# Performance work log

Measured on AMD Instinct MI355X. Metric: run time of the kernel, lower is better.

## Reference

```python
import jax, jax.numpy as jnp
import numpy as np

N = 50000      # nodes
E = 800000     # edges per relation
R = 2          # relations
L = 2          # conv layers
D = 128        # hidden / input channels
G = 64         # graphs in batch
C = 8          # num_classes


def setup_inputs() -> dict:
    key = jax.random.key(0)
    ks = jax.random.split(key, 6)
    x = jax.random.normal(ks[0], (N, D), dtype=jnp.float32)
    W = jax.random.normal(ks[1], (L, R, D, D), dtype=jnp.float32) * 0.05
    b = jnp.zeros((L, R, D), dtype=jnp.float32)
    lin_w = jax.random.normal(ks[2], (D, C), dtype=jnp.float32) * 0.05
    lin_b = jnp.zeros((C,), dtype=jnp.float32)
    edge_index = jax.random.randint(ks[3], (R, 2, E), 0, N, dtype=jnp.int32)
    batch = jnp.sort(jax.random.randint(ks[4], (N,), 0, G, dtype=jnp.int32))
    return {"x": x, "W": W, "b": b, "lin_w": lin_w, "lin_b": lin_b,
            "edge_index": edge_index, "batch": batch}


def _gcn_conv(x, src, dst, inv_sqrt_deg, W_r, b_r):
    """PyG GCNConv: symmetric-normalized aggregation with self loops.
    out[i] = sum_{j->i} d_i^-1/2 d_j^-1/2 (x_j W) + d_i^-1 (x_i W) + b
    where d includes the self loop (in-degree + 1)."""
    xw = x @ W_r                                   # [N, D]
    norm = inv_sqrt_deg[src] * inv_sqrt_deg[dst]   # [E]
    agg = jax.ops.segment_sum(xw[src] * norm[:, None], dst, num_segments=N)
    agg = agg + xw * (inv_sqrt_deg * inv_sqrt_deg)[:, None]  # self-loop msg
    return agg + b_r


def reference(x, W, b, lin_w, lin_b, edge_index, batch):
    # Pre-compute per-relation symmetric normalization (same for all layers).
    inv_sqrt_degs = []
    for r in range(R):
        dst = edge_index[r, 1]
        deg = jax.ops.segment_sum(jnp.ones((E,), x.dtype), dst, num_segments=N) + 1.0
        inv_sqrt_degs.append(jax.lax.rsqrt(deg))

    h = x
    for l in range(L):
        out = jnp.zeros((N, D), x.dtype)
        for r in range(R):  # HeteroConv aggr='sum' over relations
            out = out + _gcn_conv(h, edge_index[r, 0], edge_index[r, 1],
                                  inv_sqrt_degs[r], W[l, r], b[l, r])
        h = jax.nn.relu(out) if l < L - 1 else out

    # global_mean_pool over batch ids
    counts = jax.ops.segment_sum(jnp.ones((N,), x.dtype), batch, num_segments=G)
    sums = jax.ops.segment_sum(h, batch, num_segments=G)
    pooled = sums / jnp.maximum(counts, 1.0)[:, None]   # [G, D]
    # dropout(p=0.5) is identity in eval mode; final Linear
    return pooled @ lin_w + lin_b                        # [G, C]
```

## Files before the change

### kernel.cpp

```cpp
#include <hip/hip_runtime.h>
#include <math.h>

#define NN 50000
#define EE 800000
#define RR 2
#define LL 2
#define DD 128
#define GG 64
#define CCLS 8
#define NBUK 196
#define BCAP 6144
#define BCI2 14080

typedef unsigned int uint;
typedef unsigned short ushort;
typedef short bf16x8 __attribute__((ext_vector_type(8)));
typedef float f32x4 __attribute__((ext_vector_type(4)));
typedef float f32x2 __attribute__((ext_vector_type(2)));

#define OFF_H1    ((size_t)0)
#define OFF_WBT   ((size_t)12800000)
#define OFF_ISD   ((size_t)12931072)
#define OFF_RP    ((size_t)13331072)
#define OFF_CI    ((size_t)13732480)
#define OFF_ZERO  ((size_t)24771200)
#define OFF_BD    ((size_t)24805824)
#define OFF_XW    ((size_t)24805824)
#define ZO_GCUR 0
#define ZO_SUM  1600
#define ZO_CNT  34368
#define ZERO_BYTES 34624

static __device__ __forceinline__ ushort f2b(float f) {
  uint u = __float_as_uint(f);
  uint r = (u + 0x7fffu + ((u >> 16) & 1u)) >> 16;
  return (ushort)r;
}
static __device__ __forceinline__ float blo(uint u) { return __uint_as_float(u << 16); }
static __device__ __forceinline__ float bhi(uint u) { return __uint_as_float(u & 0xffff0000u); }

__global__ __launch_bounds__(256) void k_wprep(const float* __restrict__ W,
                                               ushort* __restrict__ WT) {
  int idx = blockIdx.x * 256 + threadIdx.x;
  int lr = idx >> 14;
  int rem = idx & 16383;
  int n = rem >> 7, k = rem & 127;
  WT[lr * 16384 + n * 128 + k] = f2b(W[lr * 16384 + k * 128 + n]);
}

__global__ __launch_bounds__(256) void k_part(const int* __restrict__ EI,
                                              int* __restrict__ gcur,
                                              uint* __restrict__ bdata) {
  __shared__ int hist[256];
  __shared__ int sbase[256];
  __shared__ int gbase[256];
  __shared__ int lcur[256];
  __shared__ uint stage[4096];
  __shared__ unsigned char bstage[4096];
  const int r = blockIdx.y;
  const int t = threadIdx.x;
  const int e0 = blockIdx.x * 4096;
  const int cnt = min(4096, EE - e0);
  hist[t] = 0;
  lcur[t] = 0;
  __syncthreads();

  int src[16], dst[16];
  bool val[4];
#pragma unroll
  for (int j = 0; j < 4; ++j) {
    int i4 = (j * 256 + t) * 4;
    val[j] = (i4 < cnt);
    if (val[j]) {
      int4 s4 = *(const int4*)(EI + (size_t)r * 2 * EE + e0 + i4);
      int4 d4 = *(const int4*)(EI + (size_t)r * 2 * EE + EE + e0 + i4);
      src[j * 4 + 0] = s4.x; src[j * 4 + 1] = s4.y; src[j * 4 + 2] = s4.z; src[j * 4 + 3] = s4.w;
      dst[j * 4 + 0] = d4.x; dst[j * 4 + 1] = d4.y; dst[j * 4 + 2] = d4.z; dst[j * 4 + 3] = d4.w;
#pragma unroll
      for (int i = 0; i < 4; ++i) atomicAdd(&hist[dst[j * 4 + i] >> 8], 1);
    }
  }
  __syncthreads();
  int hv = hist[t];
  if (t < NBUK && hv > 0)
    gbase[t] = atomicAdd(&gcur[r * NBUK + t], hv);
  else
    gbase[t] = 0;
  sbase[t] = hv;
  __syncthreads();
  for (int off = 1; off < 256; off <<= 1) {
    int u = (t >= off) ? sbase[t - off] : 0;
    __syncthreads();
    sbase[t] += u;
    __syncthreads();
  }
  int incl = sbase[t];
  hist[t] = incl - hv;
  __syncthreads();
#pragma unroll
  for (int j = 0; j < 4; ++j) {
    if (val[j]) {
#pragma unroll
      for (int i = 0; i < 4; ++i) {
        int d = dst[j * 4 + i];
        int b = d >> 8;
        int p = atomicAdd(&lcur[b], 1);
        int pos = hist[b] + p;
        stage[pos] = ((uint)src[j * 4 + i] << 8) | (uint)(d & 255);
        bstage[pos] = (unsigned char)b;
      }
    }
  }
  __syncthreads();
  for (int s = t; s < cnt; s += 256) {
    int b = (int)bstage[s];
    bdata[(size_t)(r * NBUK + b) * BCAP + gbase[b] + (s - hist[b])] = stage[s];
  }
}

__global__ __launch_bounds__(256) void k_csr(const uint* __restrict__ bdata,
                                             const int* __restrict__ gcur,
                                             float* __restrict__ isd,
                                             int* __restrict__ rps,
                                             int* __restrict__ rpc,
                                             int* __restrict__ ci) {
  __shared__ int lcnt0[256], lcnt1[256], lrp[256], lex[256], lng[256];
  __shared__ int lcurA[256], lcurB[256];
  __shared__ int cstage[BCI2];
  __shared__ int shtot;
  const int b = blockIdx.x;
  const int t = threadIdx.x;
  const int cnt0 = gcur[b];
  const int cnt1 = gcur[NBUK + b];
  const uint* bd0 = bdata + (size_t)b * BCAP;
  const uint* bd1 = bdata + (size_t)(NBUK + b) * BCAP;
  lcnt0[t] = 0; lcnt1[t] = 0; lcurA[t] = 0; lcurB[t] = 0;
  __syncthreads();
  for (int s = t; s < cnt0; s += 256) atomicAdd(&lcnt0[bd0[s] & 255u], 1);
  for (int s = t; s < cnt1; s += 256) atomicAdd(&lcnt1[bd1[s] & 255u], 1);
  __syncthreads();
  const int deg0 = lcnt0[t];
  const int deg1 = lcnt1[t];
  const int node = b * 256 + t;
  const int valid = (node < NN) ? 1 : 0;
  const int ng0 = valid ? ((deg0 + 8) >> 3) : 0;
  const int ng1 = valid ? ((deg1 + 8) >> 3) : 0;
  const int sz = (ng0 + ng1) << 3;
  lrp[t] = sz;
  __syncthreads();
  for (int off = 1; off < 256; off <<= 1) {
    int u = (t >= off) ? lrp[t - off] : 0;
    __syncthreads();
    lrp[t] += u;
    __syncthreads();
  }
  const int incl = lrp[t];
  if (t == 255) shtot = incl;
  const int ex = incl - sz;
  lex[t] = ex;
  lng[t] = ng0;
  __syncthreads();
  const int btot = shtot;
  if (t < 32) cstage[btot + t] = NN;
  rps[node] = b * BCI2 + ex;
  rpc[node] = ng0 | (ng1 << 16);
  if (valid) {
    isd[node] = rsqrtf((float)(deg0 + 1));
    isd[NN + node] = rsqrtf((float)(deg1 + 1));
    cstage[ex + deg0] = node;
    for (int p = deg0 + 1; p < (ng0 << 3); ++p) cstage[ex + p] = NN;
    const int ex1 = ex + (ng0 << 3);
    cstage[ex1 + deg1] = (NN + 1) + node;
    for (int p = deg1 + 1; p < (ng1 << 3); ++p) cstage[ex1 + p] = NN;
  }
  for (int s = t; s < cnt0; s += 256) {
    uint pr = bd0[s];
    int j = (int)(pr & 255u);
    int p = atomicAdd(&lcurA[j], 1);
    cstage[lex[j] + p] = (int)(pr >> 8);
  }
  for (int s = t; s < cnt1; s += 256) {
    uint pr = bd1[s];
    int j = (int)(pr & 255u);
    int p = atomicAdd(&lcurB[j], 1);
    cstage[lex[j] + (lng[j] << 3) + p] = (int)(pr >> 8) + (NN + 1);
  }
  __syncthreads();
  const int on = btot + 32;
  int* co = ci + (size_t)b * BCI2;
  for (int s = t; s < on; s += 256) co[s] = cstage[s];
}

#define AL_S 72
#define WT_S 136
template <int IN_BF16>
__global__ __launch_bounds__(256) void k_gemm(const void* __restrict__ Xv,
                                              const ushort* __restrict__ WTg,
                                              const float* __restrict__ isd,
                                              uint* __restrict__ Y) {
  __shared__ ushort WTl[128 * WT_S];
  __shared__ ushort Al[128 * AL_S];
  const int r = blockIdx.y;
  const int m0b = blockIdx.x * 128;
  const int t = threadIdx.x;
  const int w = t >> 6, L = t & 63, q = L >> 4, ln = L & 15;
  uint* Yr = Y + (size_t)r * (NN + 1) * 32;
  const ushort* WTr = WTg + (size_t)r * 16384;

#pragma unroll
  for (int i = 0; i < 8; ++i) {
    int g = t + i * 256;
    int n = g >> 4, k0 = (g & 15) * 8;
    *(uint4*)(&WTl[n * WT_S + k0]) = *(const uint4*)(WTr + n * 128 + k0);
  }

  f32x4 acc[2][8];
#pragma unroll
  for (int mt = 0; mt < 2; ++mt)
#pragma unroll
    for (int nt = 0; nt < 8; ++nt) {
      acc[mt][nt][0] = 0.f; acc[mt][nt][1] = 0.f;
      acc[mt][nt][2] = 0.f; acc[mt][nt][3] = 0.f;
    }

  for (int hh = 0; hh < 2; ++hh) {
    __syncthreads();
    {
      int row = t >> 1, ch = t & 1;
      int gm = m0b + row;
      ushort* dst = &Al[row * AL_S + ch * 32];
      if (gm < NN) {
        if (IN_BF16) {
          const uint4* xp = (const uint4*)((const ushort*)Xv + (size_t)gm * 128 + hh * 64 + ch * 32);
#pragma unroll
          for (int j = 0; j < 4; ++j) ((uint4*)dst)[j] = xp[j];
        } else {
          const float4* xp = (const float4*)((const float*)Xv + (size_t)gm * 128 + hh * 64 + ch * 32);
          ushort tmp[32];
#pragma unroll
          for (int j = 0; j < 8; ++j) {
            float4 v = xp[j];
            tmp[j * 4 + 0] = f2b(v.x); tmp[j * 4 + 1] = f2b(v.y);
            tmp[j * 4 + 2] = f2b(v.z); tmp[j * 4 + 3] = f2b(v.w);
          }
#pragma unroll
          for (int j = 0; j < 4; ++j) ((uint4*)dst)[j] = ((uint4*)tmp)[j];
        }
      } else {
        uint4 z = make_uint4(0, 0, 0, 0);
#pragma unroll
        for (int j = 0; j < 4; ++j) ((uint4*)dst)[j] = z;
      }
    }
    __syncthreads();
#pragma unroll
    for (int kk = 0; kk < 2; ++kk) {
      bf16x8 b0 = *(const bf16x8*)(&Al[(w * 32 + ln) * AL_S + kk * 32 + q * 8]);
      bf16x8 b1 = *(const bf16x8*)(&Al[(w * 32 + 16 + ln) * AL_S + kk * 32 + q * 8]);
#pragma unroll
      for (int nt = 0; nt < 8; ++nt) {
        bf16x8 a = *(const bf16x8*)(&WTl[(nt * 16 + ln) * WT_S + hh * 64 + kk * 32 + q * 8]);
        acc[0][nt] = __builtin_amdgcn_mfma_f32_16x16x32_bf16(a, b0, acc[0][nt], 0, 0, 0);
        acc[1][nt] = __builtin_amdgcn_mfma_f32_16x16x32_bf16(a, b1, acc[1][nt], 0, 0, 0);
      }
    }
  }
#pragma unroll
  for (int mt = 0; mt < 2; ++mt) {
    int m = m0b + w * 32 + mt * 16 + ln;
    if (m <= NN) {
      float sc = (m < NN) ? isd[r * NN + m] : 0.f;
      uint* yp = Yr + (size_t)m * 32;
#pragma unroll
      for (int nt = 0; nt < 8; ++nt) {
        f32x4 v = acc[mt][nt];
        uint u = __builtin_amdgcn_cvt_pk_fp8_f32(v[0] * sc, v[1] * sc, 0u, false);
        u = __builtin_amdgcn_cvt_pk_fp8_f32(v[2] * sc, v[3] * sc, u, true);
        yp[nt * 4 + q] = u;
      }
    }
  }
}

#define AGG_STEP()                                                           \
  {                                                                          \
    int s3 = ce0[ip]; ip += 8;                                               \
    uint4 u2 = *(const uint4*)(xw + ((size_t)((uint)s2 << 7) + cb));         \
    f32x2 v;                                                                 \
    v = __builtin_amdgcn_cvt_pk_f32_fp8(u0.x, false); acc[0] += v;           \
    v = __builtin_amdgcn_cvt_pk_f32_fp8(u0.x, true);  acc[1] += v;           \
    v = __builtin_amdgcn_cvt_pk_f32_fp8(u0.y, false); acc[2] += v;           \
    v = __builtin_amdgcn_cvt_pk_f32_fp8(u0.y, true);  acc[3] += v;           \
    v = __builtin_amdgcn_cvt_pk_f32_fp8(u0.z, false); acc[4] += v;           \
    v = __builtin_amdgcn_cvt_pk_f32_fp8(u0.z, true);  acc[5] += v;           \
    v = __builtin_amdgcn_cvt_pk_f32_fp8(u0.w, false); acc[6] += v;           \
    v = __builtin_amdgcn_cvt_pk_f32_fp8(u0.w, true);  acc[7] += v;           \
    u0 = u1; u1 = u2; s2 = s3;                                               \
  }

__global__ __launch_bounds__(256) void k_agg(const char* __restrict__ xw,
                                             const int* __restrict__ rps,
                                             const int* __restrict__ rpc,
                                             const int* __restrict__ ci,
                                             const float* __restrict__ isd,
                                             const float* __restrict__ bias,
                                             uint* __restrict__ hout, int relu_flag) {
  const int w = threadIdx.x >> 6;
  const int lane = threadIdx.x & 63;
  const int g = lane >> 3, c = lane & 7;
  const int wid = blockIdx.x * 4 + w;
  const int n0 = (wid >> 6) * 256 + (wid & 63) * 4;
  const size_t cb = (size_t)c * 16;

  const int m0 = rpc[n0], m1 = rpc[n0 + 1], m2 = rpc[n0 + 2], m3 = rpc[n0 + 3];
  const int* ce0 = ci + rps[n0];

  int ip = g;
  int s0 = ce0[ip]; ip += 8;
  int s1 = ce0[ip]; ip += 8;
  int s2 = ce0[ip]; ip += 8;
  uint4 u0 = *(const uint4*)(xw + ((size_t)((uint)s0 << 7) + cb));
  uint4 u1 = *(const uint4*)(xw + ((size_t)((uint)s1 << 7) + cb));

#pragma unroll
  for (int k = 0; k < 4; ++k) {
    const int node = n0 + k;
    const int meta_k = (k == 0) ? m0 : (k == 1) ? m1 : (k == 2) ? m2 : m3;
    const int ng0 = meta_k & 0xffff;
    const int ng1 = (meta_k >> 16) & 0xffff;
    const float di0 = isd[node];
    const float di1 = isd[NN + node];

    f32x2 acc[8];
#pragma unroll
    for (int j = 0; j < 8; ++j) { acc[j][0] = 0.f; acc[j][1] = 0.f; }
    for (int q = 0; q < ng0; ++q) AGG_STEP();
    f32x2 t8[8];
    {
      f32x2 d; d[0] = di0; d[1] = di0;
#pragma unroll
      for (int j = 0; j < 8; ++j) { t8[j] = acc[j] * d; acc[j][0] = 0.f; acc[j][1] = 0.f; }
    }
    for (int q = 0; q < ng1; ++q) AGG_STEP();
    {
      f32x2 d; d[0] = di1; d[1] = di1;
#pragma unroll
      for (int j = 0; j < 8; ++j) t8[j] += acc[j] * d;
    }

#pragma unroll
    for (int mask = 8; mask <= 32; mask <<= 1) {
#pragma unroll
      for (int j = 0; j < 8; ++j) {
        f32x2 o;
        o[0] = __shfl_xor(t8[j][0], mask);
        o[1] = __shfl_xor(t8[j][1], mask);
        t8[j] += o;
      }
    }

    if (g == 0 && node < NN) {
      const float4* p0 = (const float4*)(bias + c * 16);
      const float4* p1 = (const float4*)(bias + DD + c * 16);
      float o[16];
#pragma unroll
      for (int j = 0; j < 4; ++j) {
        float4 a = p0[j], bq = p1[j];
        o[4 * j + 0] = t8[2 * j][0] + a.x + bq.x;
        o[4 * j + 1] = t8[2 * j][1] + a.y + bq.y;
        o[4 * j + 2] = t8[2 * j + 1][0] + a.z + bq.z;
        o[4 * j + 3] = t8[2 * j + 1][1] + a.w + bq.w;
      }
      if (relu_flag) {
#pragma unroll
        for (int j = 0; j < 16; ++j) o[j] = fmaxf(o[j], 0.f);
      }
      uint pk[8];
#pragma unroll
      for (int j = 0; j < 8; ++j)
        pk[j] = (uint)f2b(o[2 * j]) | ((uint)f2b(o[2 * j + 1]) << 16);
      uint4* dst = (uint4*)(hout + (size_t)node * 64) + c * 2;
      dst[0] = make_uint4(pk[0], pk[1], pk[2], pk[3]);
      dst[1] = make_uint4(pk[4], pk[5], pk[6], pk[7]);
    }
  }
}

#define PCHUNK 32
__global__ __launch_bounds__(64) void k_pool(const uint* __restrict__ h,
                                             const int* __restrict__ batch,
                                             float* __restrict__ sums,
                                             int* __restrict__ counts) {
  int lane = threadIdx.x;
  int n0 = blockIdx.x * PCHUNK;
  int n1 = n0 + PCHUNK;
  if (n1 > NN) n1 = NN;
  if (n0 >= NN) return;
  float aLo = 0.f, aHi = 0.f;
  int cnt = 0;
  int g = batch[n0];
  uint u = h[(size_t)n0 * 64 + lane];
  for (int n = n0; n < n1; ++n) {
    uint unext = 0;
    int gnext = g;
    if (n + 1 < n1) {
      unext = h[(size_t)(n + 1) * 64 + lane];
      gnext = batch[n + 1];
    }
    aLo += blo(u);
    aHi += bhi(u);
    cnt++;
    if (n + 1 < n1 && gnext != g) {
      atomicAdd(&sums[g * DD + lane * 2], aLo);
      atomicAdd(&sums[g * DD + lane * 2 + 1], aHi);
      if (lane == 0) atomicAdd(&counts[g], cnt);
      aLo = 0.f; aHi = 0.f; cnt = 0;
      g = gnext;
    }
    u = unext;
  }
  atomicAdd(&sums[g * DD + lane * 2], aLo);
  atomicAdd(&sums[g * DD + lane * 2 + 1], aHi);
  if (lane == 0) atomicAdd(&counts[g], cnt);
}

__global__ __launch_bounds__(512) void k_final(const float* __restrict__ sums,
                                               const int* __restrict__ counts,
                                               const float* __restrict__ lin_w,
                                               const float* __restrict__ lin_b,
                                               float* __restrict__ out) {
  int t = threadIdx.x;
  int g = t >> 3, co = t & 7;
  float cnt = (float)counts[g];
  if (cnt < 1.f) cnt = 1.f;
  float inv = 1.f / cnt;
  float v = lin_b[co];
  for (int d = 0; d < DD; ++d) v += (sums[g * DD + d] * inv) * lin_w[d * CCLS + co];
  out[t] = v;
}

extern "C" void kernel_launch(void* const* d_in, const int* in_sizes, int n_in,
                              void* d_out, int out_size, void* d_ws, size_t ws_size,
                              hipStream_t stream) {
  (void)in_sizes; (void)n_in; (void)out_size; (void)ws_size;
  const float* x     = (const float*)d_in[0];
  const float* W     = (const float*)d_in[1];
  const float* b     = (const float*)d_in[2];
  const float* lin_w = (const float*)d_in[3];
  const float* lin_b = (const float*)d_in[4];
  const int*   EI    = (const int*)d_in[5];
  const int*   batch = (const int*)d_in[6];
  float* out = (float*)d_out;

  char* ws = (char*)d_ws;
  uint*   h1    = (uint*)(ws + OFF_H1);
  ushort* WbfT  = (ushort*)(ws + OFF_WBT);
  float*  isd   = (float*)(ws + OFF_ISD);
  int*    rps   = (int*)(ws + OFF_RP);
  int*    rpc   = rps + NBUK * 256;
  int*    ci    = (int*)(ws + OFF_CI);
  uint*   bdata = (uint*)(ws + OFF_BD);
  uint*   xw    = (uint*)(ws + OFF_XW);
  char*   zb    = ws + OFF_ZERO;
  int*    gcur  = (int*)(zb + ZO_GCUR);
  float*  sums  = (float*)(zb + ZO_SUM);
  int*    counts= (int*)(zb + ZO_CNT);

  (void)hipMemsetAsync(zb, 0, ZERO_BYTES, stream);

  k_wprep<<<256, 256, 0, stream>>>(W, WbfT);
  k_part<<<dim3((EE + 4095) / 4096, RR), 256, 0, stream>>>(EI, gcur, bdata);
  k_csr<<<NBUK, 256, 0, stream>>>(bdata, gcur, isd, rps, rpc, ci);

  for (int l = 0; l < LL; ++l) {
    const ushort* WTl_g = WbfT + (size_t)l * RR * DD * DD;
    if (l == 0)
      k_gemm<0><<<dim3((NN + 127) / 128, RR), 256, 0, stream>>>((const void*)x, WTl_g, isd, xw);
    else
      k_gemm<1><<<dim3((NN + 127) / 128, RR), 256, 0, stream>>>((const void*)h1, WTl_g, isd, xw);
    k_agg<<<(NBUK * 64) / 4, 256, 0, stream>>>((const char*)xw, rps, rpc, ci, isd,
                                               b + (size_t)l * RR * DD, h1,
                                               (l < LL - 1) ? 1 : 0);
  }
  k_pool<<<(NN + PCHUNK - 1) / PCHUNK, 64, 0, stream>>>(h1, batch, sums, counts);
  k_final<<<1, GG * CCLS, 0, stream>>>(sums, counts, lin_w, lin_b, out);
}
```

Baseline: 288.1 us.

## Merge per-relation CSR padding and assign one node per wavefront in aggregation

The CSR builder now packs both relations' neighbour lists for a node contiguously, padding only the combined list to a multiple of 8 instead of padding each relation separately. This cuts wasted dummy gathers. The aggregation kernel now gives each wavefront a single node instead of four. It applies the per-relation normalisation per slot using the relation boundary, launches four times as many blocks, and sets an occupancy hint. This is meant to improve load balance and latency hiding, at the cost of an extra multiply per element and per-slot select logic, and of losing prefetch carry-over across nodes.

```diff
diff --git a/kernel.cpp b/kernel.cpp
--- a/kernel.cpp
+++ b/kernel.cpp
@@ -124,7 +124,7 @@
                                              int* __restrict__ rps,
                                              int* __restrict__ rpc,
                                              int* __restrict__ ci) {
-  __shared__ int lcnt0[256], lcnt1[256], lrp[256], lex[256], lng[256];
+  __shared__ int lcnt0[256], lcnt1[256], lrp[256], lex[256], lend0[256];
   __shared__ int lcurA[256], lcurB[256];
   __shared__ int cstage[BCI2];
   __shared__ int shtot;
@@ -143,9 +143,10 @@
   const int deg1 = lcnt1[t];
   const int node = b * 256 + t;
   const int valid = (node < NN) ? 1 : 0;
-  const int ng0 = valid ? ((deg0 + 8) >> 3) : 0;
-  const int ng1 = valid ? ((deg1 + 8) >> 3) : 0;
-  const int sz = (ng0 + ng1) << 3;
+  const int nreal = deg0 + deg1 + 2;
+  const int ng = valid ? ((nreal + 7) >> 3) : 0;
+  const int sz = ng << 3;
+  const int end0 = deg0 + 1;
   lrp[t] = sz;
   __syncthreads();
   for (int off = 1; off < 256; off <<= 1) {
@@ -158,20 +159,18 @@
   if (t == 255) shtot = incl;
   const int ex = incl - sz;
   lex[t] = ex;
-  lng[t] = ng0;
+  lend0[t] = end0;
   __syncthreads();
   const int btot = shtot;
   if (t < 32) cstage[btot + t] = NN;
   rps[node] = b * BCI2 + ex;
-  rpc[node] = ng0 | (ng1 << 16);
+  rpc[node] = valid ? (ng | (end0 << 16)) : 0;
   if (valid) {
     isd[node] = rsqrtf((float)(deg0 + 1));
     isd[NN + node] = rsqrtf((float)(deg1 + 1));
     cstage[ex + deg0] = node;
-    for (int p = deg0 + 1; p < (ng0 << 3); ++p) cstage[ex + p] = NN;
-    const int ex1 = ex + (ng0 << 3);
-    cstage[ex1 + deg1] = (NN + 1) + node;
-    for (int p = deg1 + 1; p < (ng1 << 3); ++p) cstage[ex1 + p] = NN;
+    cstage[ex + end0 + deg1] = (NN + 1) + node;
+    for (int p = end0 + deg1 + 1; p < sz; ++p) cstage[ex + p] = NN;
   }
   for (int s = t; s < cnt0; s += 256) {
     uint pr = bd0[s];
@@ -183,7 +182,7 @@
     uint pr = bd1[s];
     int j = (int)(pr & 255u);
     int p = atomicAdd(&lcurB[j], 1);
-    cstage[lex[j] + (lng[j] << 3) + p] = (int)(pr >> 8) + (NN + 1);
+    cstage[lex[j] + lend0[j] + p] = (int)(pr >> 8) + (NN + 1);
   }
   __syncthreads();
   const int on = btot + 32;
@@ -282,107 +281,92 @@
   }
 }
 
-#define AGG_STEP()                                                           \
-  {                                                                          \
-    int s3 = ce0[ip]; ip += 8;                                               \
-    uint4 u2 = *(const uint4*)(xw + ((size_t)((uint)s2 << 7) + cb));         \
-    f32x2 v;                                                                 \
-    v = __builtin_amdgcn_cvt_pk_f32_fp8(u0.x, false); acc[0] += v;           \
-    v = __builtin_amdgcn_cvt_pk_f32_fp8(u0.x, true);  acc[1] += v;           \
-    v = __builtin_amdgcn_cvt_pk_f32_fp8(u0.y, false); acc[2] += v;           \
-    v = __builtin_amdgcn_cvt_pk_f32_fp8(u0.y, true);  acc[3] += v;           \
-    v = __builtin_amdgcn_cvt_pk_f32_fp8(u0.z, false); acc[4] += v;           \
-    v = __builtin_amdgcn_cvt_pk_f32_fp8(u0.z, true);  acc[5] += v;           \
-    v = __builtin_amdgcn_cvt_pk_f32_fp8(u0.w, false); acc[6] += v;           \
-    v = __builtin_amdgcn_cvt_pk_f32_fp8(u0.w, true);  acc[7] += v;           \
-    u0 = u1; u1 = u2; s2 = s3;                                               \
-  }
-
-__global__ __launch_bounds__(256) void k_agg(const char* __restrict__ xw,
-                                             const int* __restrict__ rps,
-                                             const int* __restrict__ rpc,
-                                             const int* __restrict__ ci,
-                                             const float* __restrict__ isd,
-                                             const float* __restrict__ bias,
-                                             uint* __restrict__ hout, int relu_flag) {
+__global__ __launch_bounds__(256, 6) void k_agg(const char* __restrict__ xw,
+                                                const int* __restrict__ rps,
+                                                const int* __restrict__ rpc,
+                                                const int* __restrict__ ci,
+                                                const float* __restrict__ isd,
+                                                const float* __restrict__ bias,
+                                                uint* __restrict__ hout, int relu_flag) {
   const int w = threadIdx.x >> 6;
   const int lane = threadIdx.x & 63;
   const int g = lane >> 3, c = lane & 7;
-  const int wid = blockIdx.x * 4 + w;
-  const int n0 = (wid >> 6) * 256 + (wid & 63) * 4;
+  const int node = blockIdx.x * 4 + w;
   const size_t cb = (size_t)c * 16;
 
-  const int m0 = rpc[n0], m1 = rpc[n0 + 1], m2 = rpc[n0 + 2], m3 = rpc[n0 + 3];
-  const int* ce0 = ci + rps[n0];
+  const int meta = rpc[node];
+  const int ng = meta & 0xffff;
+  const int end0 = (meta >> 16) & 0xffff;
+  const int lim = ng << 3;
+  const int* ce = ci + rps[node];
+  const float di0 = isd[node < NN ? node : 0];
+  const float di1 = isd[NN + (node < NN ? node : 0)];
 
   int ip = g;
-  int s0 = ce0[ip]; ip += 8;
-  int s1 = ce0[ip]; ip += 8;
-  int s2 = ce0[ip]; ip += 8;
-  uint4 u0 = *(const uint4*)(xw + ((size_t)((uint)s0 << 7) + cb));
-  uint4 u1 = *(const uint4*)(xw + ((size_t)((uint)s1 << 7) + cb));
-
-#pragma unroll
-  for (int k = 0; k < 4; ++k) {
-    const int node = n0 + k;
-    const int meta_k = (k == 0) ? m0 : (k == 1) ? m1 : (k == 2) ? m2 : m3;
-    const int ng0 = meta_k & 0xffff;
-    const int ng1 = (meta_k >> 16) & 0xffff;
-    const float di0 = isd[node];
-    const float di1 = isd[NN + node];
-
-    f32x2 acc[8];
-#pragma unroll
-    for (int j = 0; j < 8; ++j) { acc[j][0] = 0.f; acc[j][1] = 0.f; }
-    for (int q = 0; q < ng0; ++q) AGG_STEP();
-    f32x2 t8[8];
-    {
-      f32x2 d; d[0] = di0; d[1] = di0;
-#pragma unroll
-      for (int j = 0; j < 8; ++j) { t8[j] = acc[j] * d; acc[j][0] = 0.f; acc[j][1] = 0.f; }
-    }
-    for (int q = 0; q < ng1; ++q) AGG_STEP();
-    {
-      f32x2 d; d[0] = di1; d[1] = di1;
-#pragma unroll
-      for (int j = 0; j < 8; ++j) t8[j] += acc[j] * d;
-    }
-
-#pragma unroll
-    for (int mask = 8; mask <= 32; mask <<= 1) {
-#pragma unroll
-      for (int j = 0; j < 8; ++j) {
-        f32x2 o;
-        o[0] = __shfl_xor(t8[j][0], mask);
-        o[1] = __shfl_xor(t8[j][1], mask);
-        t8[j] += o;
-      }
-    }
-
-    if (g == 0 && node < NN) {
-      const float4* p0 = (const float4*)(bias + c * 16);
-      const float4* p1 = (const float4*)(bias + DD + c * 16);
-      float o[16];
-#pragma unroll
-      for (int j = 0; j < 4; ++j) {
-        float4 a = p0[j], bq = p1[j];
-        o[4 * j + 0] = t8[2 * j][0] + a.x + bq.x;
-        o[4 * j + 1] = t8[2 * j][1] + a.y + bq.y;
-        o[4 * j + 2] = t8[2 * j + 1][0] + a.z + bq.z;
-        o[4 * j + 3] = t8[2 * j + 1][1] + a.w + bq.w;
-      }
-      if (relu_flag) {
-#pragma unroll
-        for (int j = 0; j < 16; ++j) o[j] = fmaxf(o[j], 0.f);
-      }
-      uint pk[8];
-#pragma unroll
-      for (int j = 0; j < 8; ++j)
-        pk[j] = (uint)f2b(o[2 * j]) | ((uint)f2b(o[2 * j + 1]) << 16);
-      uint4* dst = (uint4*)(hout + (size_t)node * 64) + c * 2;
-      dst[0] = make_uint4(pk[0], pk[1], pk[2], pk[3]);
-      dst[1] = make_uint4(pk[4], pk[5], pk[6], pk[7]);
-    }
+  int s0 = ce[ip]; s0 = (ip < lim) ? s0 : NN; ip += 8;
+  uint4 d0 = *(const uint4*)(xw + (((size_t)(uint)s0 << 7) + cb));
+  int s1 = ce[ip]; s1 = (ip < lim) ? s1 : NN; ip += 8;
+  uint4 d1 = *(const uint4*)(xw + (((size_t)(uint)s1 << 7) + cb));
+  int s2 = ce[ip]; s2 = (ip < lim) ? s2 : NN; ip += 8;
+  uint4 d2 = *(const uint4*)(xw + (((size_t)(uint)s2 << 7) + cb));
+
+  f32x2 acc[8];
+#pragma unroll
+  for (int j = 0; j < 8; ++j) { acc[j][0] = 0.f; acc[j][1] = 0.f; }
+
+  int slotc = g;
+  for (int q = 0; q < ng; ++q) {
+    int s3 = ce[ip]; s3 = (ip < lim) ? s3 : NN; ip += 8;
+    uint4 d3 = *(const uint4*)(xw + (((size_t)(uint)s3 << 7) + cb));
+    const float sc = (slotc < end0) ? di0 : di1;
+    slotc += 8;
+    f32x2 sc2; sc2[0] = sc; sc2[1] = sc;
+    f32x2 v;
+    v = __builtin_amdgcn_cvt_pk_f32_fp8(d0.x, false); acc[0] += v * sc2;
+    v = __builtin_amdgcn_cvt_pk_f32_fp8(d0.x, true);  acc[1] += v * sc2;
+    v = __builtin_amdgcn_cvt_pk_f32_fp8(d0.y, false); acc[2] += v * sc2;
+    v = __builtin_amdgcn_cvt_pk_f32_fp8(d0.y, true);  acc[3] += v * sc2;
+    v = __builtin_amdgcn_cvt_pk_f32_fp8(d0.z, false); acc[4] += v * sc2;
+    v = __builtin_amdgcn_cvt_pk_f32_fp8(d0.z, true);  acc[5] += v * sc2;
+    v = __builtin_amdgcn_cvt_pk_f32_fp8(d0.w, false); acc[6] += v * sc2;
+    v = __builtin_amdgcn_cvt_pk_f32_fp8(d0.w, true);  acc[7] += v * sc2;
+    d0 = d1; d1 = d2; d2 = d3;
+  }
+
+#pragma unroll
+  for (int mask = 8; mask <= 32; mask <<= 1) {
+#pragma unroll
+    for (int j = 0; j < 8; ++j) {
+      f32x2 o;
+      o[0] = __shfl_xor(acc[j][0], mask);
+      o[1] = __shfl_xor(acc[j][1], mask);
+      acc[j] += o;
+    }
+  }
+
+  if (g == 0 && node < NN) {
+    const float4* p0 = (const float4*)(bias + c * 16);
+    const float4* p1 = (const float4*)(bias + DD + c * 16);
+    float o[16];
+#pragma unroll
+    for (int j = 0; j < 4; ++j) {
+      float4 a = p0[j], bq = p1[j];
+      o[4 * j + 0] = acc[2 * j][0] + a.x + bq.x;
+      o[4 * j + 1] = acc[2 * j][1] + a.y + bq.y;
+      o[4 * j + 2] = acc[2 * j + 1][0] + a.z + bq.z;
+      o[4 * j + 3] = acc[2 * j + 1][1] + a.w + bq.w;
+    }
+    if (relu_flag) {
+#pragma unroll
+      for (int j = 0; j < 16; ++j) o[j] = fmaxf(o[j], 0.f);
+    }
+    uint pk[8];
+#pragma unroll
+    for (int j = 0; j < 8; ++j)
+      pk[j] = (uint)f2b(o[2 * j]) | ((uint)f2b(o[2 * j + 1]) << 16);
+    uint4* dst = (uint4*)(hout + (size_t)node * 64) + c * 2;
+    dst[0] = make_uint4(pk[0], pk[1], pk[2], pk[3]);
+    dst[1] = make_uint4(pk[4], pk[5], pk[6], pk[7]);
   }
 }
 
@@ -478,9 +462,9 @@
       k_gemm<0><<<dim3((NN + 127) / 128, RR), 256, 0, stream>>>((const void*)x, WTl_g, isd, xw);
     else
       k_gemm<1><<<dim3((NN + 127) / 128, RR), 256, 0, stream>>>((const void*)h1, WTl_g, isd, xw);
-    k_agg<<<(NBUK * 64) / 4, 256, 0, stream>>>((const char*)xw, rps, rpc, ci, isd,
-                                               b + (size_t)l * RR * DD, h1,
-                                               (l < LL - 1) ? 1 : 0);
+    k_agg<<<(NBUK * 256) / 4, 256, 0, stream>>>((const char*)xw, rps, rpc, ci, isd,
+                                                b + (size_t)l * RR * DD, h1,
+                                                (l < LL - 1) ? 1 : 0);
   }
   k_pool<<<(NN + PCHUNK - 1) / PCHUNK, 64, 0, stream>>>(h1, batch, sums, counts);
   k_final<<<1, GG * CCLS, 0, stream>>>(sums, counts, lin_w, lin_b, out);
```

Result: faster. 272.7 us (-5.3%).
